# Kernel optimization log

Measured on AMD Instinct MI355X. Metric: run time of the kernel, lower is better.

## Reference

```python
import jax, jax.numpy as jnp
import numpy as np

T, B, C = 4096, 8, 1024
H, K = 16, 31


def setup_inputs() -> dict:
    key = jax.random.key(0)
    k1, k2 = jax.random.split(key)
    x = jax.random.normal(k1, (T, B, C), dtype=jnp.float32)
    # kaiming-uniform-ish init on (H, 1, K)
    bound = float(np.sqrt(6.0 / K))
    weight = jax.random.uniform(k2, (H, 1, K), dtype=jnp.float32, minval=-bound, maxval=bound)
    return {"x": x, "weight": weight}


def reference(x, weight):
    # x: (T, B, C); weight: (H, 1, K) shared across R = C // H channels per head.
    T_, B_, C_ = x.shape
    H_, _, K_ = weight.shape
    R = C_ // H_
    pad_l = K_ // 2  # calc_padding for odd K
    # Expand head weights to per-channel depthwise filters: (C, 1, K)
    w = jnp.repeat(weight, R, axis=0)
    xb = jnp.transpose(x, (1, 2, 0))  # (B, C, T)
    # out[t] = sum_k w[k] * x[t - pad_l + k]  (cross-correlation, matching unfold1d)
    out = jax.lax.conv_general_dilated(
        xb, w,
        window_strides=(1,),
        padding=[(pad_l, K_ - 1 - pad_l)],
        feature_group_count=C_,
        dimension_numbers=("NCH", "OIH", "NCH"),
    )  # (B, C, T)
    return jnp.transpose(out, (2, 0, 1))  # (T, B, C)
```

## Files before the change

kernel.cpp:

```cpp
#include <hip/hip_runtime.h>


#define T_DIM 4096
#define B_DIM 8
#define C_DIM 1024
#define H_DIM 16
#define K_DIM 31
#define PAD   15
#define ROWS  (B_DIM * C_DIM)
#define S_LEN 128
#define CH    16

__global__ __launch_bounds__(256, 2)
void lconv_kernel(const float* __restrict__ x,
                  const float* __restrict__ w,
                  float* __restrict__ out) {
    __shared__ float lw[H_DIM * K_DIM];
    const int tid = threadIdx.x;
    for (int i = tid; i < H_DIM * K_DIM; i += 256) lw[i] = w[i];
    __syncthreads();

    const int idx = blockIdx.x * 256 + tid;
    const int h   = (idx & (C_DIM - 1)) >> 6;

    float wk[K_DIM];
    #pragma unroll
    for (int k = 0; k < K_DIM; ++k) {
        wk[k] = __uint_as_float(
            __builtin_amdgcn_readfirstlane(__float_as_uint(lw[h * K_DIM + k])));
    }

    const int t0 = blockIdx.y * S_LEN;

    float win[K_DIM - 1 + CH];

    #pragma unroll
    for (int i = 0; i < K_DIM - 1; ++i) {
        const int t = t0 - PAD + i;
        win[i] = (t >= 0) ? x[(size_t)t * ROWS + idx] : 0.0f;
    }

    for (int cb = 0; cb < S_LEN / CH; ++cb) {
        const int tb = t0 + cb * CH;

        #pragma unroll
        for (int j = 0; j < CH; ++j) {
            const int t = tb + PAD + j;
            win[K_DIM - 1 + j] = (t < T_DIM) ? x[(size_t)t * ROWS + idx] : 0.0f;
        }

        #pragma unroll
        for (int j = 0; j < CH; ++j) {
            float acc = 0.0f;
            #pragma unroll
            for (int k = 0; k < K_DIM; ++k)
                acc = fmaf(wk[k], win[j + k], acc);
            out[(size_t)(tb + j) * ROWS + idx] = acc;
        }

        #pragma unroll
        for (int i = 0; i < K_DIM - 1; ++i) win[i] = win[i + CH];
    }
}

extern "C" void kernel_launch(void* const* d_in, const int* in_sizes, int n_in,
                              void* d_out, int out_size, void* d_ws, size_t ws_size,
                              hipStream_t stream) {
    const float* x = (const float*)d_in[0];
    const float* w = (const float*)d_in[1];
    float* out = (float*)d_out;

    dim3 grid(ROWS / 256, T_DIM / S_LEN);
    lconv_kernel<<<grid, 256, 0, stream>>>(x, w, out);
}
```

Before: 242.7 us.

## Split time axis into one 16-step chunk per block and load full window upfront

Each block now processes a single 16-step time chunk instead of a 128-step strip, increasing the grid size and loading the whole 46-element window at once with a fast unguarded path for interior chunks. This removes the serial chunk loop and window shifting, aiming for more parallelism and memory-level parallelism. The cost is re-reading the 30-row halo per 16 outputs, which substantially increases input traffic (partly absorbed by cache). The launch bounds occupancy hint is also dropped.

```diff
diff --git a/kernel.cpp b/kernel.cpp
--- a/kernel.cpp
+++ b/kernel.cpp
@@ -8,10 +8,10 @@
 #define K_DIM 31
 #define PAD   15
 #define ROWS  (B_DIM * C_DIM)
-#define S_LEN 128
 #define CH    16
+#define WIN   (K_DIM - 1 + CH)
 
-__global__ __launch_bounds__(256, 2)
+__global__ __launch_bounds__(256)
 void lconv_kernel(const float* __restrict__ x,
                   const float* __restrict__ w,
                   float* __restrict__ out) {
@@ -30,36 +30,31 @@
             __builtin_amdgcn_readfirstlane(__float_as_uint(lw[h * K_DIM + k])));
     }
 
-    const int t0 = blockIdx.y * S_LEN;
+    const int t0 = blockIdx.y * CH;
+    const float* xp = x + (long long)(t0 - PAD) * ROWS + idx;
 
-    float win[K_DIM - 1 + CH];
+    float win[WIN];
 
-    #pragma unroll
-    for (int i = 0; i < K_DIM - 1; ++i) {
-        const int t = t0 - PAD + i;
-        win[i] = (t >= 0) ? x[(size_t)t * ROWS + idx] : 0.0f;
+    if (t0 >= PAD && t0 + CH + PAD <= T_DIM) {
+        #pragma unroll
+        for (int i = 0; i < WIN; ++i)
+            win[i] = xp[(long long)i * ROWS];
+    } else {
+        #pragma unroll
+        for (int i = 0; i < WIN; ++i) {
+            const int t = t0 - PAD + i;
+            win[i] = (t >= 0 && t < T_DIM) ? xp[(long long)i * ROWS] : 0.0f;
+        }
     }
 
-    for (int cb = 0; cb < S_LEN / CH; ++cb) {
-        const int tb = t0 + cb * CH;
-
+    float* op = out + (long long)t0 * ROWS + idx;
+    #pragma unroll
+    for (int j = 0; j < CH; ++j) {
+        float acc = 0.0f;
         #pragma unroll
-        for (int j = 0; j < CH; ++j) {
-            const int t = tb + PAD + j;
-            win[K_DIM - 1 + j] = (t < T_DIM) ? x[(size_t)t * ROWS + idx] : 0.0f;
-        }
-
-        #pragma unroll
-        for (int j = 0; j < CH; ++j) {
-            float acc = 0.0f;
-            #pragma unroll
-            for (int k = 0; k < K_DIM; ++k)
-                acc = fmaf(wk[k], win[j + k], acc);
-            out[(size_t)(tb + j) * ROWS + idx] = acc;
-        }
-
-        #pragma unroll
-        for (int i = 0; i < K_DIM - 1; ++i) win[i] = win[i + CH];
+        for (int k = 0; k < K_DIM; ++k)
+            acc = fmaf(wk[k], win[j + k], acc);
+        op[(long long)j * ROWS] = acc;
     }
 }
 
@@ -70,6 +65,6 @@
     const float* w = (const float*)d_in[1];
     float* out = (float*)d_out;
 
-    dim3 grid(ROWS / 256, T_DIM / S_LEN);
+    dim3 grid(ROWS / 256, T_DIM / CH);
     lconv_kernel<<<grid, 256, 0, stream>>>(x, w, out);
 }
```

After: 232.5 us. 4.2% less time.
